# Kernel optimization log

Hardware: AMD Instinct MI355X
Metric: run time of the kernel (lower is better)

Reference implementation:

```python
import jax, jax.numpy as jnp
import numpy as np

N_NODES = 50000
N_EDGES = 640000
D_IN = 128
D_OUT = 128


def setup_inputs() -> dict:
    key = jax.random.key(0)
    k1, k2, k3, k4, k5 = jax.random.split(key, 5)
    features = jax.random.normal(k1, (N_NODES, D_IN), dtype=jnp.float32)
    src = jax.random.randint(k2, (N_EDGES,), 0, N_NODES, dtype=jnp.int64)
    dst = jax.random.randint(k3, (N_EDGES,), 0, N_NODES, dtype=jnp.int64)
    W = jax.random.normal(k4, (D_IN, D_OUT), dtype=jnp.float32)
    b = jax.random.normal(k5, (1, D_OUT), dtype=jnp.float32)
    return {"features": features, "src": src, "dst": dst, "W": W, "b": b}


def reference(features, src, dst, W, b):
    # ptens.gather: sum neighbor features into each destination node
    msgs = features[src]                                  # [E, D_IN] gathered edge messages
    agg = jax.ops.segment_sum(msgs, dst, num_segments=N_NODES)  # [N, D_IN]
    # Linear: x @ W + b
    return agg @ W + b
```

## Files before the change

### kernel.cpp

```cpp
#include <hip/hip_runtime.h>

#define N_NODES 50000
#define N_EDGES 640000
#define D 128
#define NBINS 392
#define NCHUNK 96
#define NQUADS 160000
#define EPC4 1667
#define BINCAP 2048


typedef __attribute__((ext_vector_type(8))) short short8;
typedef __attribute__((ext_vector_type(4))) float f32x4;

static __device__ inline unsigned pkbf(float lo, float hi) {
    unsigned a = __float_as_uint(lo) + 0x8000u;
    unsigned b = __float_as_uint(hi) + 0x8000u;
    return __builtin_amdgcn_perm(b, a, 0x07060302);
}
static __device__ inline unsigned short f2bf(float f) {
    return (unsigned short)((__float_as_uint(f) + 0x8000u) >> 16);
}
static __device__ inline float bflo(unsigned u) { return __uint_as_float(u << 16); }
static __device__ inline float bfhi(unsigned u) { return __uint_as_float(u & 0xFFFF0000u); }

__global__ __launch_bounds__(1024) void hist_kernel(
        const int4* __restrict__ dst4,
        const float* __restrict__ W,
        uint4* __restrict__ Wf,
        unsigned* __restrict__ hist) {
    __shared__ unsigned h[NBINS];
    const int t = threadIdx.x;
    const int blk = blockIdx.x;
    if (t < NBINS) h[t] = 0;

    if (blk < 2) {
        int e = blk * 1024 + t;
        int q  = e & 3;
        int n  = (e >> 2) & 15;
        int nt = (e >> 6) & 7;
        int kt = e >> 9;
        const float* p = W + (kt * 32 + q * 8) * D + nt * 16 + n;
        unsigned u[8];
        #pragma unroll
        for (int j = 0; j < 8; ++j) u[j] = __float_as_uint(p[j * D]) + 0x8000u;
        uint4 o;
        o.x = __builtin_amdgcn_perm(u[1], u[0], 0x07060302);
        o.y = __builtin_amdgcn_perm(u[3], u[2], 0x07060302);
        o.z = __builtin_amdgcn_perm(u[5], u[4], 0x07060302);
        o.w = __builtin_amdgcn_perm(u[7], u[6], 0x07060302);
        Wf[e] = o;
    }
    __syncthreads();

    const int i0 = blk * EPC4;
    const int i1 = min(i0 + EPC4, NQUADS);
    for (int i = i0 + t; i < i1; i += 1024) {
        int4 d = dst4[i];
        atomicAdd(&h[((unsigned)d.x) >> 7], 1u);
        atomicAdd(&h[((unsigned)d.y) >> 7], 1u);
        atomicAdd(&h[((unsigned)d.z) >> 7], 1u);
        atomicAdd(&h[((unsigned)d.w) >> 7], 1u);
    }
    __syncthreads();
    if (t < NBINS) hist[blk * NBINS + t] = h[t];
}

__global__ __launch_bounds__(1024) void scatter_kernel(
        const int4* __restrict__ src4,
        const int4* __restrict__ dst4,
        const unsigned* __restrict__ hist,
        unsigned* __restrict__ recs,
        unsigned* __restrict__ binbase) {
    __shared__ unsigned sc[512];
    __shared__ unsigned lb[NBINS];
    __shared__ unsigned h[NBINS];
    const int t = threadIdx.x;
    const int blk = blockIdx.x;

    unsigned pre = 0, tot = 0;
    if (t < NBINS)
        for (int k = 0; k < NCHUNK; ++k) {
            unsigned v = hist[k * NBINS + t];
            if (k < blk) pre += v;
            tot += v;
        }
    if (t < 512) sc[t] = (t < NBINS) ? tot : 0;
    __syncthreads();
    for (int off = 1; off < 512; off <<= 1) {
        unsigned v = 0;
        if (t < 512) { v = sc[t]; if (t >= off) v += sc[t - off]; }
        __syncthreads();
        if (t < 512) sc[t] = v;
        __syncthreads();
    }
    if (t < NBINS) {
        unsigned bbs = (t == 0) ? 0u : sc[t - 1];
        lb[t] = bbs + pre;
        h[t] = 0;
        if (blk == 0) binbase[t] = bbs;
    }
    if (blk == 0 && t == NBINS) binbase[NBINS] = N_EDGES;
    __syncthreads();

    const int i0 = blk * EPC4;
    const int i1 = min(i0 + EPC4, NQUADS);
    for (int i = i0 + t; i < i1; i += 1024) {
        int4 s = src4[i];
        int4 d = dst4[i];
        #pragma unroll
        for (int u = 0; u < 4; ++u) {
            int dd = (u == 0) ? d.x : (u == 1) ? d.y : (u == 2) ? d.z : d.w;
            int ss = (u == 0) ? s.x : (u == 1) ? s.y : (u == 2) ? s.z : s.w;
            unsigned bin = ((unsigned)dd) >> 7;
            unsigned r = atomicAdd(&h[bin], 1u);
            unsigned off = lb[bin] + r;
            if (off < N_EDGES)
                recs[off] = (((unsigned)dd) << 16) | (unsigned)ss;
        }
    }
}

__global__ __launch_bounds__(256) void gemm_kernel(
        const uint4* __restrict__ Wf,
        const float* __restrict__ feat,
        unsigned short* __restrict__ Y) {
    const int t = threadIdx.x;
    const int tile = blockIdx.x;
    const int wave = t >> 6;
    const int lane = t & 63;
    const int n = lane & 15;
    const int q = lane >> 4;

    short8 bfrag[4][2];
    #pragma unroll
    for (int kt = 0; kt < 4; ++kt) {
        #pragma unroll
        for (int p = 0; p < 2; ++p) {
            int nt = wave * 2 + p;
            uint4 raw = Wf[(((kt * 8 + nt) * 16 + n) << 2) + q];
            bfrag[kt][p] = *(const short8*)&raw;
        }
    }

    const float* ap = feat + (size_t)(tile * 16 + n) * D + q * 8;
    f32x4 acc0 = {0.f, 0.f, 0.f, 0.f};
    f32x4 acc1 = {0.f, 0.f, 0.f, 0.f};
    #pragma unroll
    for (int kt = 0; kt < 4; ++kt) {
        float4 f0 = *(const float4*)(ap + kt * 32);
        float4 f1 = *(const float4*)(ap + kt * 32 + 4);
        int4 pa;
        pa.x = (int)pkbf(f0.x, f0.y);
        pa.y = (int)pkbf(f0.z, f0.w);
        pa.z = (int)pkbf(f1.x, f1.y);
        pa.w = (int)pkbf(f1.z, f1.w);
        short8 afrag = *(const short8*)&pa;
        acc0 = __builtin_amdgcn_mfma_f32_16x16x32_bf16(afrag, bfrag[kt][0], acc0, 0, 0, 0);
        acc1 = __builtin_amdgcn_mfma_f32_16x16x32_bf16(afrag, bfrag[kt][1], acc1, 0, 0, 0);
    }
    unsigned short* yp = Y + (size_t)(tile * 16 + q * 4) * D + n;
    #pragma unroll
    for (int i = 0; i < 4; ++i) {
        yp[(size_t)i * D + wave * 32]      = f2bf(acc0[i]);
        yp[(size_t)i * D + wave * 32 + 16] = f2bf(acc1[i]);
    }
}

__global__ __launch_bounds__(512) void nodesort_kernel(
        const unsigned* __restrict__ binbase,
        const unsigned* __restrict__ recs,
        unsigned* __restrict__ nodeoff,
        unsigned short* __restrict__ edst) {
    __shared__ unsigned lrec[BINCAP];
    __shared__ unsigned cnt128[128];
    __shared__ unsigned ns[129];
    __shared__ unsigned tick[128];
    const int t = threadIdx.x;
    const int b = blockIdx.x;
    const unsigned s0 = binbase[b];
    const unsigned e1 = binbase[b + 1];
    unsigned n = e1 - s0;
    if (n > BINCAP) n = BINCAP;
    if (t < 128) cnt128[t] = 0;
    __syncthreads();
    for (unsigned i = t; i < n; i += 512) {
        unsigned r = recs[s0 + i];
        lrec[i] = r;
        atomicAdd(&cnt128[(r >> 16) & 127u], 1u);
    }
    __syncthreads();
    if (t == 0) {
        unsigned a = 0;
        for (int i = 0; i < 128; ++i) { ns[i] = a; a += cnt128[i]; }
        ns[128] = a;
    }
    __syncthreads();
    if (t < 128) {
        tick[t] = ns[t];
        nodeoff[b * 128 + t] = s0 + ns[t];
    }
    if (b == 0 && t == 128) nodeoff[NBINS * 128] = N_EDGES;
    __syncthreads();
    for (unsigned i = t; i < n; i += 512) {
        unsigned r = lrec[i];
        unsigned off = s0 + atomicAdd(&tick[(r >> 16) & 127u], 1u);
        edst[off] = (unsigned short)(r & 0xFFFFu);
    }
}

#define ACC8(v)                                              \
    do {                                                     \
        ax[0] += bflo((v).x); ax[1] += bfhi((v).x);          \
        ax[2] += bflo((v).y); ax[3] += bfhi((v).y);          \
        ax[4] += bflo((v).z); ax[5] += bfhi((v).z);          \
        ax[6] += bflo((v).w); ax[7] += bfhi((v).w);          \
    } while (0)

__global__ __launch_bounds__(256) void gather_kernel(
        const uint4* __restrict__ Y4,
        const unsigned* __restrict__ nodeoff,
        const unsigned short* __restrict__ edst,
        const float4* __restrict__ b4,
        float* __restrict__ out) {
    int node = (blockIdx.x * 256 + threadIdx.x) >> 6;
    int lane = threadIdx.x & 63;
    if (node >= N_NODES) return;
    unsigned start = nodeoff[node];
    int cnt = (int)(nodeoff[node + 1] - start);
    const int q = lane >> 4;
    const int c = lane & 15;

    float ax[8];
    #pragma unroll
    for (int i = 0; i < 8; ++i) ax[i] = 0.f;

    for (int c0 = 0; c0 < cnt; c0 += 64) {
        int m = min(cnt - c0, 64);
        int eid = (lane < m) ? (int)edst[start + c0 + lane] : 0;
        for (int j = 0; j < m; j += 16) {
            int i0 = j + q, i1 = j + 4 + q, i2 = j + 8 + q, i3 = j + 12 + q;
            int s0 = __shfl(eid, i0 & 63);
            int s1 = __shfl(eid, i1 & 63);
            int s2 = __shfl(eid, i2 & 63);
            int s3 = __shfl(eid, i3 & 63);
            uint4 v0 = Y4[(size_t)s0 * 16 + c];
            uint4 v1 = Y4[(size_t)s1 * 16 + c];
            uint4 v2 = Y4[(size_t)s2 * 16 + c];
            uint4 v3 = Y4[(size_t)s3 * 16 + c];
            v0.x = (i0 < m) ? v0.x : 0u; v0.y = (i0 < m) ? v0.y : 0u;
            v0.z = (i0 < m) ? v0.z : 0u; v0.w = (i0 < m) ? v0.w : 0u;
            v1.x = (i1 < m) ? v1.x : 0u; v1.y = (i1 < m) ? v1.y : 0u;
            v1.z = (i1 < m) ? v1.z : 0u; v1.w = (i1 < m) ? v1.w : 0u;
            v2.x = (i2 < m) ? v2.x : 0u; v2.y = (i2 < m) ? v2.y : 0u;
            v2.z = (i2 < m) ? v2.z : 0u; v2.w = (i2 < m) ? v2.w : 0u;
            v3.x = (i3 < m) ? v3.x : 0u; v3.y = (i3 < m) ? v3.y : 0u;
            v3.z = (i3 < m) ? v3.z : 0u; v3.w = (i3 < m) ? v3.w : 0u;
            ACC8(v0);
            ACC8(v1);
            ACC8(v2);
            ACC8(v3);
        }
    }

    #pragma unroll
    for (int i = 0; i < 8; ++i) {
        ax[i] += __shfl_xor(ax[i], 16);
        ax[i] += __shfl_xor(ax[i], 32);
    }

    if (lane < 32) {
        int q2 = lane >> 4;
        float4 bb = b4[c * 2 + q2];
        float4 o;
        o.x = ax[q2 * 4 + 0] + bb.x;
        o.y = ax[q2 * 4 + 1] + bb.y;
        o.z = ax[q2 * 4 + 2] + bb.z;
        o.w = ax[q2 * 4 + 3] + bb.w;
        *(float4*)(out + (size_t)node * D + c * 8 + q2 * 4) = o;
    }
}

extern "C" void kernel_launch(void* const* d_in, const int* in_sizes, int n_in,
                              void* d_out, int out_size, void* d_ws, size_t ws_size,
                              hipStream_t stream) {
    const float* feat = (const float*)d_in[0];
    const int*   src  = (const int*)d_in[1];
    const int*   dst  = (const int*)d_in[2];
    const float* W    = (const float*)d_in[3];
    const float* b    = (const float*)d_in[4];
    float* out = (float*)d_out;

    unsigned short* Y = (unsigned short*)d_ws;
    uint4* Wf = (uint4*)((char*)d_ws + (size_t)N_NODES * D * 2);
    unsigned* hist    = (unsigned*)((char*)Wf + 2048 * sizeof(uint4));
    unsigned* binbase = hist + NCHUNK * NBINS;
    unsigned* nodeoff = binbase + (NBINS + 1);
    unsigned* recs    = nodeoff + (NBINS * 128 + 1);
    unsigned short* edst = (unsigned short*)(recs + N_EDGES);

    hist_kernel<<<NCHUNK, 1024, 0, stream>>>((const int4*)dst, W, Wf, hist);
    scatter_kernel<<<NCHUNK, 1024, 0, stream>>>(
        (const int4*)src, (const int4*)dst, hist, recs, binbase);
    gemm_kernel<<<3125, 256, 0, stream>>>(Wf, feat, Y);
    nodesort_kernel<<<NBINS, 512, 0, stream>>>(binbase, recs, nodeoff, edst);
    gather_kernel<<<N_NODES * 64 / 256, 256, 0, stream>>>(
        (const uint4*)Y, nodeoff, edst, (const float4*)b, out);
}
```

Baseline: 145.3 us.

## Split Y into four column planes and gather one plane per pass

The GEMM output is stored as four separate column planes of 32 bf16 each, written per wave, instead of one row-major array. The gather launches four times as many blocks, each handling one plane, so every plane (about 3.2 MB) is more likely to stay resident in cache during its random-access reads. The cost is that the edge lists and node offsets are read four times, and each load is narrower (4 bytes per lane instead of 16), which means more load instructions per byte fetched.

```diff
diff --git a/kernel.cpp b/kernel.cpp
--- a/kernel.cpp
+++ b/kernel.cpp
@@ -8,6 +8,9 @@
 #define NQUADS 160000
 #define EPC4 1667
 #define BINCAP 2048
+#define GBLOCKS 12500
+#define PLANE_U (N_NODES*16)
+#define PLANE_H (N_NODES*32)
 
 
 typedef __attribute__((ext_vector_type(8))) short short8;
@@ -124,7 +127,7 @@
 __global__ __launch_bounds__(256) void gemm_kernel(
         const uint4* __restrict__ Wf,
         const float* __restrict__ feat,
-        unsigned short* __restrict__ Y) {
+        unsigned short* __restrict__ Yq) {
     const int t = threadIdx.x;
     const int tile = blockIdx.x;
     const int wave = t >> 6;
@@ -159,11 +162,12 @@
         acc0 = __builtin_amdgcn_mfma_f32_16x16x32_bf16(afrag, bfrag[kt][0], acc0, 0, 0, 0);
         acc1 = __builtin_amdgcn_mfma_f32_16x16x32_bf16(afrag, bfrag[kt][1], acc1, 0, 0, 0);
     }
-    unsigned short* yp = Y + (size_t)(tile * 16 + q * 4) * D + n;
+    unsigned short* yp = Yq + (size_t)wave * PLANE_H
+                            + (size_t)(tile * 16 + q * 4) * 32 + n;
     #pragma unroll
     for (int i = 0; i < 4; ++i) {
-        yp[(size_t)i * D + wave * 32]      = f2bf(acc0[i]);
-        yp[(size_t)i * D + wave * 32 + 16] = f2bf(acc1[i]);
+        yp[i * 32]      = f2bf(acc0[i]);
+        yp[i * 32 + 16] = f2bf(acc1[i]);
     }
 }
 
@@ -209,32 +213,23 @@
     }
 }
 
-#define ACC8(v)                                              \
-    do {                                                     \
-        ax[0] += bflo((v).x); ax[1] += bfhi((v).x);          \
-        ax[2] += bflo((v).y); ax[3] += bfhi((v).y);          \
-        ax[4] += bflo((v).z); ax[5] += bfhi((v).z);          \
-        ax[6] += bflo((v).w); ax[7] += bfhi((v).w);          \
-    } while (0)
-
 __global__ __launch_bounds__(256) void gather_kernel(
-        const uint4* __restrict__ Y4,
+        const unsigned* __restrict__ Yq,
         const unsigned* __restrict__ nodeoff,
         const unsigned short* __restrict__ edst,
-        const float4* __restrict__ b4,
+        const float* __restrict__ b,
         float* __restrict__ out) {
-    int node = (blockIdx.x * 256 + threadIdx.x) >> 6;
-    int lane = threadIdx.x & 63;
-    if (node >= N_NODES) return;
-    unsigned start = nodeoff[node];
-    int cnt = (int)(nodeoff[node + 1] - start);
+    const int pass = blockIdx.x / GBLOCKS;
+    const int blk  = blockIdx.x - pass * GBLOCKS;
+    const int node = (blk * 256 + (int)threadIdx.x) >> 6;
+    const int lane = threadIdx.x & 63;
+    const unsigned start = nodeoff[node];
+    const int cnt = (int)(nodeoff[node + 1] - start);
     const int q = lane >> 4;
     const int c = lane & 15;
-
-    float ax[8];
-    #pragma unroll
-    for (int i = 0; i < 8; ++i) ax[i] = 0.f;
-
+    const unsigned* Yp = Yq + (size_t)pass * PLANE_U;
+
+    float ax0 = 0.f, ax1 = 0.f;
     for (int c0 = 0; c0 < cnt; c0 += 64) {
         int m = min(cnt - c0, 64);
         int eid = (lane < m) ? (int)edst[start + c0 + lane] : 0;
@@ -244,40 +239,30 @@
             int s1 = __shfl(eid, i1 & 63);
             int s2 = __shfl(eid, i2 & 63);
             int s3 = __shfl(eid, i3 & 63);
-            uint4 v0 = Y4[(size_t)s0 * 16 + c];
-            uint4 v1 = Y4[(size_t)s1 * 16 + c];
-            uint4 v2 = Y4[(size_t)s2 * 16 + c];
-            uint4 v3 = Y4[(size_t)s3 * 16 + c];
-            v0.x = (i0 < m) ? v0.x : 0u; v0.y = (i0 < m) ? v0.y : 0u;
-            v0.z = (i0 < m) ? v0.z : 0u; v0.w = (i0 < m) ? v0.w : 0u;
-            v1.x = (i1 < m) ? v1.x : 0u; v1.y = (i1 < m) ? v1.y : 0u;
-            v1.z = (i1 < m) ? v1.z : 0u; v1.w = (i1 < m) ? v1.w : 0u;
-            v2.x = (i2 < m) ? v2.x : 0u; v2.y = (i2 < m) ? v2.y : 0u;
-            v2.z = (i2 < m) ? v2.z : 0u; v2.w = (i2 < m) ? v2.w : 0u;
-            v3.x = (i3 < m) ? v3.x : 0u; v3.y = (i3 < m) ? v3.y : 0u;
-            v3.z = (i3 < m) ? v3.z : 0u; v3.w = (i3 < m) ? v3.w : 0u;
-            ACC8(v0);
-            ACC8(v1);
-            ACC8(v2);
-            ACC8(v3);
-        }
-    }
-
-    #pragma unroll
-    for (int i = 0; i < 8; ++i) {
-        ax[i] += __shfl_xor(ax[i], 16);
-        ax[i] += __shfl_xor(ax[i], 32);
-    }
-
-    if (lane < 32) {
-        int q2 = lane >> 4;
-        float4 bb = b4[c * 2 + q2];
-        float4 o;
-        o.x = ax[q2 * 4 + 0] + bb.x;
-        o.y = ax[q2 * 4 + 1] + bb.y;
-        o.z = ax[q2 * 4 + 2] + bb.z;
-        o.w = ax[q2 * 4 + 3] + bb.w;
-        *(float4*)(out + (size_t)node * D + c * 8 + q2 * 4) = o;
+            unsigned v0 = Yp[(size_t)s0 * 16 + c];
+            unsigned v1 = Yp[(size_t)s1 * 16 + c];
+            unsigned v2 = Yp[(size_t)s2 * 16 + c];
+            unsigned v3 = Yp[(size_t)s3 * 16 + c];
+            v0 = (i0 < m) ? v0 : 0u;
+            v1 = (i1 < m) ? v1 : 0u;
+            v2 = (i2 < m) ? v2 : 0u;
+            v3 = (i3 < m) ? v3 : 0u;
+            ax0 += bflo(v0) + bflo(v1) + bflo(v2) + bflo(v3);
+            ax1 += bfhi(v0) + bfhi(v1) + bfhi(v2) + bfhi(v3);
+        }
+    }
+
+    ax0 += __shfl_xor(ax0, 16);
+    ax0 += __shfl_xor(ax0, 32);
+    ax1 += __shfl_xor(ax1, 16);
+    ax1 += __shfl_xor(ax1, 32);
+
+    if (lane < 16) {
+        int col = pass * 32 + 2 * c;
+        float2 o;
+        o.x = ax0 + b[col];
+        o.y = ax1 + b[col + 1];
+        *(float2*)(out + (size_t)node * D + col) = o;
     }
 }
 
@@ -291,7 +276,7 @@
     const float* b    = (const float*)d_in[4];
     float* out = (float*)d_out;
 
-    unsigned short* Y = (unsigned short*)d_ws;
+    unsigned short* Yq = (unsigned short*)d_ws;
     uint4* Wf = (uint4*)((char*)d_ws + (size_t)N_NODES * D * 2);
     unsigned* hist    = (unsigned*)((char*)Wf + 2048 * sizeof(uint4));
     unsigned* binbase = hist + NCHUNK * NBINS;
@@ -302,8 +287,8 @@
     hist_kernel<<<NCHUNK, 1024, 0, stream>>>((const int4*)dst, W, Wf, hist);
     scatter_kernel<<<NCHUNK, 1024, 0, stream>>>(
         (const int4*)src, (const int4*)dst, hist, recs, binbase);
-    gemm_kernel<<<3125, 256, 0, stream>>>(Wf, feat, Y);
+    gemm_kernel<<<3125, 256, 0, stream>>>(Wf, feat, Yq);
     nodesort_kernel<<<NBINS, 512, 0, stream>>>(binbase, recs, nodeoff, edst);
-    gather_kernel<<<N_NODES * 64 / 256, 256, 0, stream>>>(
-        (const uint4*)Y, nodeoff, edst, (const float4*)b, out);
-}
+    gather_kernel<<<4 * GBLOCKS, 256, 0, stream>>>(
+        (const unsigned*)Yq, nodeoff, edst, b, out);
+}
```

Measured after the change: 173.7 us. 19.5% more time.
